# Optimization experiments

Measured on AMD Instinct MI355X. Metric: run time of the kernel, lower is better.

## Reference

```python
import jax, jax.numpy as jnp
import numpy as np

LN_EPS = 1e-5


def setup_inputs() -> dict:
    key = jax.random.key(0)
    ks = jax.random.split(key, 8)
    dim = 256
    b, n3 = 8, 6144  # seq dim holds 3 concatenated token streams of n=2048 each
    s = 0.02
    return {
        "x": jax.random.normal(ks[0], (b, n3, dim), jnp.float32),
        "ln_g": jnp.ones((dim,), jnp.float32),
        "ln_b": jnp.zeros((dim,), jnp.float32),
        "Wq": jax.random.normal(ks[1], (dim, dim), jnp.float32) * s,
        "bq": jax.random.normal(ks[2], (dim,), jnp.float32) * s,
        "Wk": jax.random.normal(ks[3], (dim, dim), jnp.float32) * s,
        "bk": jax.random.normal(ks[4], (dim,), jnp.float32) * s,
        "Wv": jax.random.normal(ks[5], (dim, dim), jnp.float32) * s,
        "bv": jax.random.normal(ks[6], (dim,), jnp.float32) * s,
        "Wo": jax.random.normal(ks[7], (dim, dim), jnp.float32) * s,
        "bo": jnp.zeros((dim,), jnp.float32),
        "heads": 8,
    }


def reference(x, ln_g, ln_b, Wq, bq, Wk, bk, Wv, bv, Wo, bo, heads):
    dim = x.shape[-1]
    scale = dim ** (-0.5)  # NOTE: full dim, as in the original module
    d = dim // heads

    def cross_attn(xcat):
        # LayerNorm over last dim (applied to concatenated [2b, n, dim])
        mu = jnp.mean(xcat, axis=-1, keepdims=True)
        var = jnp.mean(jnp.square(xcat - mu), axis=-1, keepdims=True)
        xn = (xcat - mu) * jax.lax.rsqrt(var + LN_EPS) * ln_g + ln_b
        x1, x2 = jnp.split(xn, 2, axis=0)  # queries from stream 1, kv from stream 2
        q = x1 @ Wq.T + bq
        k = x2 @ Wk.T + bk
        v = x2 @ Wv.T + bv
        b_, n_ = q.shape[0], q.shape[1]
        q = q.reshape(b_, n_, heads, d).transpose(0, 2, 1, 3)  # b h n d
        k = k.reshape(b_, n_, heads, d).transpose(0, 2, 1, 3)
        v = v.reshape(b_, n_, heads, d).transpose(0, 2, 1, 3)
        dots = jnp.einsum('bhid,bhjd->bhij', q, k) * scale
        attn = jax.nn.softmax(dots, axis=-1)
        out = jnp.einsum('bhij,bhjd->bhid', attn, v)
        out = out.transpose(0, 2, 1, 3).reshape(b_, n_, dim)
        return out @ Wo.T + bo  # dropout is identity in eval

    x_origin, x_emap, x_lbp = jnp.split(x, 3, axis=1)
    out_oe = cross_attn(jnp.concatenate((x_origin, x_emap), axis=0))
    out_ol = cross_attn(jnp.concatenate((x_origin, x_lbp), axis=0))
    return out_oe + out_ol
```

## Files before the change

### kernel.cpp

```cpp
#include <hip/hip_runtime.h>
#include <hip/hip_bf16.h>
#include <math.h>

#define LN_EPS 1e-5f
#define QSCALE 0.09016844005556021f

typedef __attribute__((ext_vector_type(8))) short short8;
typedef __attribute__((ext_vector_type(4))) short short4v;
typedef __attribute__((ext_vector_type(4))) float f32x4;
typedef __attribute__((ext_vector_type(16))) float f32x16;

__device__ inline ushort f2bf(float f) {
  __hip_bfloat16 h = __float2bfloat16(f);
  return *reinterpret_cast<ushort*>(&h);
}

__device__ inline uint pk2bf(float a, float b) {
  uint ua = __float_as_uint(a) + 0x8000u;
  uint ub = __float_as_uint(b) + 0x8000u;
  return __builtin_amdgcn_perm(ub, ua, 0x07060302u);
}


__global__ __launch_bounds__(256) void ln_wcast_kernel(
    const float* __restrict__ x, const float* __restrict__ lng,
    const float* __restrict__ lnb,
    const float* __restrict__ Wq, const float* __restrict__ Wk,
    const float* __restrict__ Wv, const float* __restrict__ Wo,
    ushort* __restrict__ xn, ushort* __restrict__ wbf) {
  if (blockIdx.x < 256) {
    int t = blockIdx.x * 256 + threadIdx.x;
    int e0 = t * 4;
    int m = e0 >> 16, off = e0 & 65535;
    const float* src = (m == 0) ? Wq : (m == 1) ? Wk : (m == 2) ? Wv : Wo;
    float4 v = *(const float4*)(src + off);
    ushort4 o;
    o.x = f2bf(v.x); o.y = f2bf(v.y); o.z = f2bf(v.z); o.w = f2bf(v.w);
    *(ushort4*)(wbf + m * 65536 + off) = o;
    return;
  }
  int w = threadIdx.x >> 6;
  int lane = threadIdx.x & 63;
  size_t token = (size_t)(blockIdx.x - 256) * 4 + w;
  float4 v = *(const float4*)(x + token * 256 + lane * 4);
  float s  = v.x + v.y + v.z + v.w;
  float s2 = v.x * v.x + v.y * v.y + v.z * v.z + v.w * v.w;
#pragma unroll
  for (int off = 32; off >= 1; off >>= 1) {
    s  += __shfl_xor(s, off, 64);
    s2 += __shfl_xor(s2, off, 64);
  }
  float mu  = s * (1.0f / 256.0f);
  float var = s2 * (1.0f / 256.0f) - mu * mu;
  float rs  = rsqrtf(var + LN_EPS);
  float4 g = *(const float4*)(lng + lane * 4);
  float4 bb = *(const float4*)(lnb + lane * 4);
  ushort4 o;
  o.x = f2bf((v.x - mu) * rs * g.x + bb.x);
  o.y = f2bf((v.y - mu) * rs * g.y + bb.y);
  o.z = f2bf((v.z - mu) * rs * g.z + bb.z);
  o.w = f2bf((v.w - mu) * rs * g.w + bb.w);
  *(ushort4*)(xn + token * 256 + lane * 4) = o;
}

__global__ __launch_bounds__(256) void proj_kernel(
    const ushort* __restrict__ xn,
    const ushort* __restrict__ wq, const ushort* __restrict__ wk,
    const ushort* __restrict__ wv,
    const float* __restrict__ bq, const float* __restrict__ bk,
    const float* __restrict__ bv,
    ushort* __restrict__ qb, ushort* __restrict__ keb, ushort* __restrict__ vTe,
    ushort* __restrict__ klb, ushort* __restrict__ vTl) {
  int z = blockIdx.z;
  int tid = threadIdx.x;
  int w = tid >> 6, lane = tid & 63;
  int n = lane & 15, quad = lane >> 4;
  int cbase = blockIdx.y * 128 + w * 32;
  int b = (blockIdx.x * 128) >> 11;
  int r0 = (blockIdx.x * 128) & 2047;

  if (z == 0) {
    const ushort* xbase = xn + ((size_t)b * 6144 + r0) * 256;
    short8 wf[2][8];
#pragma unroll
    for (int ct = 0; ct < 2; ++ct)
#pragma unroll
      for (int kc = 0; kc < 8; ++kc)
        wf[ct][kc] = *(const short8*)(wq + (size_t)(cbase + ct * 16 + n) * 256 + kc * 32 + quad * 8);
    float4 bt[2];
    bt[0] = *(const float4*)(bq + cbase + quad * 4);
    bt[1] = *(const float4*)(bq + cbase + 16 + quad * 4);

    short8 xfA[8], xfB[8];
#pragma unroll
    for (int kc = 0; kc < 8; ++kc)
      xfA[kc] = *(const short8*)(xbase + (size_t)n * 256 + kc * 32 + quad * 8);

#pragma unroll
    for (int tt = 0; tt < 8; ++tt) {
      const short8* cur = (tt & 1) ? xfB : xfA;
      short8* nxt = (tt & 1) ? xfA : xfB;
      if (tt < 7) {
#pragma unroll
        for (int kc = 0; kc < 8; ++kc)
          nxt[kc] = *(const short8*)(xbase + (size_t)((tt + 1) * 16 + n) * 256 + kc * 32 + quad * 8);
      }
      f32x4 acc[2] = {{0.f, 0.f, 0.f, 0.f}, {0.f, 0.f, 0.f, 0.f}};
#pragma unroll
      for (int ct = 0; ct < 2; ++ct)
#pragma unroll
        for (int kc = 0; kc < 8; ++kc)
          acc[ct] = __builtin_amdgcn_mfma_f32_16x16x32_bf16(wf[ct][kc], cur[kc], acc[ct], 0, 0, 0);
      int n2 = r0 + tt * 16 + n;
#pragma unroll
      for (int ct = 0; ct < 2; ++ct) {
        int c = cbase + ct * 16 + quad * 4;
        int h = c >> 5, d = c & 31;
        float* bp = (float*)&bt[ct];
        ushort4 st;
        st.x = f2bf((acc[ct][0] + bp[0]) * QSCALE);
        st.y = f2bf((acc[ct][1] + bp[1]) * QSCALE);
        st.z = f2bf((acc[ct][2] + bp[2]) * QSCALE);
        st.w = f2bf((acc[ct][3] + bp[3]) * QSCALE);
        *(ushort4*)(qb + (((size_t)(b * 8 + h) * 2048) + n2) * 32 + d) = st;
      }
    }
  } else {
    int s = z;
    ushort* kout = (z == 1) ? keb : klb;
    ushort* vout = (z == 1) ? vTe : vTl;
    const ushort* xbase = xn + ((size_t)b * 6144 + s * 2048 + r0) * 256;
    short8 wfk[2][8], wfv[2][8];
#pragma unroll
    for (int ct = 0; ct < 2; ++ct)
#pragma unroll
      for (int kc = 0; kc < 8; ++kc) {
        wfk[ct][kc] = *(const short8*)(wk + (size_t)(cbase + ct * 16 + n) * 256 + kc * 32 + quad * 8);
        wfv[ct][kc] = *(const short8*)(wv + (size_t)(cbase + ct * 16 + n) * 256 + kc * 32 + quad * 8);
      }
    float4 btk[2];
    btk[0] = *(const float4*)(bk + cbase + quad * 4);
    btk[1] = *(const float4*)(bk + cbase + 16 + quad * 4);
    float bsv[2] = {bv[cbase + n], bv[cbase + 16 + n]};

    short8 xfA[8], xfB[8];
#pragma unroll
    for (int kc = 0; kc < 8; ++kc)
      xfA[kc] = *(const short8*)(xbase + (size_t)n * 256 + kc * 32 + quad * 8);

#pragma unroll
    for (int tt = 0; tt < 8; ++tt) {
      const short8* cur = (tt & 1) ? xfB : xfA;
      short8* nxt = (tt & 1) ? xfA : xfB;
      if (tt < 7) {
#pragma unroll
        for (int kc = 0; kc < 8; ++kc)
          nxt[kc] = *(const short8*)(xbase + (size_t)((tt + 1) * 16 + n) * 256 + kc * 32 + quad * 8);
      }
      f32x4 ack[2] = {{0.f, 0.f, 0.f, 0.f}, {0.f, 0.f, 0.f, 0.f}};
      f32x4 acv[2] = {{0.f, 0.f, 0.f, 0.f}, {0.f, 0.f, 0.f, 0.f}};
#pragma unroll
      for (int ct = 0; ct < 2; ++ct)
#pragma unroll
        for (int kc = 0; kc < 8; ++kc) {
          ack[ct] = __builtin_amdgcn_mfma_f32_16x16x32_bf16(wfk[ct][kc], cur[kc], ack[ct], 0, 0, 0);
          acv[ct] = __builtin_amdgcn_mfma_f32_16x16x32_bf16(cur[kc], wfv[ct][kc], acv[ct], 0, 0, 0);
        }
      int n2 = r0 + tt * 16 + n;
#pragma unroll
      for (int ct = 0; ct < 2; ++ct) {
        int c = cbase + ct * 16 + quad * 4;
        int h = c >> 5, d = c & 31;
        float* bp = (float*)&btk[ct];
        ushort4 st;
        st.x = f2bf(ack[ct][0] + bp[0]);
        st.y = f2bf(ack[ct][1] + bp[1]);
        st.z = f2bf(ack[ct][2] + bp[2]);
        st.w = f2bf(ack[ct][3] + bp[3]);
        *(ushort4*)(kout + (((size_t)(b * 8 + h) * 2048) + n2) * 32 + d) = st;
      }
      int tq = r0 + tt * 16 + quad * 4;
      int ktile = tq >> 5;
      int u = (tq >> 4) & 1;
      int i0 = 4 * (quad >> 1);
      int hi2 = quad & 1;
#pragma unroll
      for (int ct = 0; ct < 2; ++ct) {
        int c = cbase + ct * 16 + n;
        int h = c >> 5;
        int d = ct * 16 + n;
        int lane2 = d + 32 * hi2;
        ushort4 st;
        st.x = f2bf(acv[ct][0] + bsv[ct]);
        st.y = f2bf(acv[ct][1] + bsv[ct]);
        st.z = f2bf(acv[ct][2] + bsv[ct]);
        st.w = f2bf(acv[ct][3] + bsv[ct]);
        *(ushort4*)(vout + (size_t)(b * 8 + h) * 65536
                    + ktile * 1024 + u * 512 + lane2 * 8 + i0) = st;
      }
    }
  }
}

__global__ __launch_bounds__(256, 3) void attn_kernel(
    const ushort* __restrict__ q,
    const ushort* __restrict__ ke, const ushort* __restrict__ vTe,
    const ushort* __restrict__ kl, const ushort* __restrict__ vTl,
    ushort* __restrict__ osum_e, ushort* __restrict__ osum_l) {
  int tid = threadIdx.x;
  int w = tid >> 6, lane = tid & 63;
  int l31 = lane & 31, hi = lane >> 5;

  union { uint4 uu; short8 s8; } one_u;
  one_u.uu.x = 0x3F803F80u; one_u.uu.y = 0x3F803F80u;
  one_u.uu.z = 0x3F803F80u; one_u.uu.w = 0x3F803F80u;
  const short8 vone8 = one_u.s8;

  int L = blockIdx.y * 8 + blockIdx.x;
  int xcd = L & 7, idx = L >> 3;
  int bh = (idx >> 5) * 8 + xcd;
  int rem = idx & 31;
  int s = rem >> 4;
  int q0 = (rem & 15) * 128;
  int qbase = q0 + w * 32;

  const ushort* K  = (s == 0 ? ke : kl) + (size_t)bh * 65536;
  const ushort* VT = (s == 0 ? vTe : vTl) + (size_t)bh * 65536;
  ushort* osum = (s == 0) ? osum_e : osum_l;

  short8 qf[2];
#pragma unroll
  for (int sl = 0; sl < 2; ++sl)
    qf[sl] = *(const short8*)(q + ((size_t)bh * 2048 + qbase + l31) * 32 + sl * 16 + hi * 8);

  f32x16 zero16;
#pragma unroll
  for (int r = 0; r < 16; ++r) zero16[r] = 0.f;
  f32x16 oacc = zero16;
  f32x16 lacc = zero16;

  auto loadKV = [&](short8* kf, short8* vf, int jt) {
    const ushort* kb = K + (size_t)jt * 2048;
#pragma unroll
    for (int kt = 0; kt < 2; ++kt)
#pragma unroll
      for (int sl = 0; sl < 2; ++sl)
        kf[kt * 2 + sl] = *(const short8*)(kb + (kt * 32 + l31) * 32 + sl * 16 + hi * 8);
    const ushort* vb = VT + (size_t)jt * 2048 + lane * 8;
#pragma unroll
    for (int m = 0; m < 4; ++m)
      vf[m] = *(const short8*)(vb + m * 512);
  };

  auto compute = [&](const short8* kf, const short8* vf) {
#pragma unroll
    for (int kt = 0; kt < 2; ++kt) {
      __builtin_amdgcn_s_setprio(1);
      f32x16 sacc = __builtin_amdgcn_mfma_f32_32x32x16_bf16(kf[kt * 2 + 0], qf[0], zero16, 0, 0, 0);
      sacc = __builtin_amdgcn_mfma_f32_32x32x16_bf16(kf[kt * 2 + 1], qf[1], sacc, 0, 0, 0);
      __builtin_amdgcn_s_setprio(0);
      float p[16];
#pragma unroll
      for (int r = 0; r < 16; ++r) p[r] = __builtin_amdgcn_exp2f(sacc[r]);
      short8 pa[2];
#pragma unroll
      for (int u = 0; u < 2; ++u) {
        union { uint4 uu; short8 s8; } cv;
        cv.uu.x = pk2bf(p[8 * u + 0], p[8 * u + 1]);
        cv.uu.y = pk2bf(p[8 * u + 2], p[8 * u + 3]);
        cv.uu.z = pk2bf(p[8 * u + 4], p[8 * u + 5]);
        cv.uu.w = pk2bf(p[8 * u + 6], p[8 * u + 7]);
        pa[u] = cv.s8;
      }
      __builtin_amdgcn_s_setprio(1);
      oacc = __builtin_amdgcn_mfma_f32_32x32x16_bf16(pa[0], vf[kt * 2 + 0], oacc, 0, 0, 0);
      oacc = __builtin_amdgcn_mfma_f32_32x32x16_bf16(pa[1], vf[kt * 2 + 1], oacc, 0, 0, 0);
      lacc = __builtin_amdgcn_mfma_f32_32x32x16_bf16(pa[0], vone8, lacc, 0, 0, 0);
      lacc = __builtin_amdgcn_mfma_f32_32x32x16_bf16(pa[1], vone8, lacc, 0, 0, 0);
      __builtin_amdgcn_s_setprio(0);
    }
  };

  short8 kfA[4], kfB[4], vfA[4], vfB[4];
  loadKV(kfA, vfA, 0);
  for (int jt = 0; jt < 32; jt += 2) {
    loadKV(kfB, vfB, jt + 1);
    compute(kfA, vfA);
    if (jt + 2 < 32) loadKV(kfA, vfA, jt + 2);
    compute(kfB, vfB);
  }

  int b = bh >> 3, h = bh & 7;
#pragma unroll
  for (int r = 0; r < 16; ++r) {
    int qr = (r & 3) + 8 * (r >> 2) + 4 * hi;
    float invr = __builtin_amdgcn_rcpf(lacc[r]);
    float v = oacc[r] * invr;
    size_t row = (size_t)b * 2048 + qbase + qr;
    osum[row * 256 + h * 32 + l31] = f2bf(v);
  }
}

__global__ __launch_bounds__(256) void outproj_kernel(
    const ushort* __restrict__ ose, const ushort* __restrict__ osl,
    const ushort* __restrict__ wo,
    const float* __restrict__ bo, float* __restrict__ out) {
  int tid = threadIdx.x;
  int w = tid >> 6, lane = tid & 63;
  int n = lane & 15, quad = lane >> 4;
  int cbase = blockIdx.y * 128 + w * 32;

  short8 wfrag[2][8];
#pragma unroll
  for (int ct = 0; ct < 2; ++ct)
#pragma unroll
    for (int kc = 0; kc < 8; ++kc)
      wfrag[ct][kc] = *(const short8*)(wo + (size_t)(cbase + ct * 16 + n) * 256 + kc * 32 + quad * 8);
  float4 bt[2];
  bt[0] = *(const float4*)(bo + cbase + quad * 4);
  bt[1] = *(const float4*)(bo + cbase + 16 + quad * 4);

  const ushort* ae = ose + (size_t)(blockIdx.x * 64) * 256;
  const ushort* al = osl + (size_t)(blockIdx.x * 64) * 256;

#pragma unroll
  for (int tt = 0; tt < 4; ++tt) {
    short8 xe[8], xl[8];
#pragma unroll
    for (int kc = 0; kc < 8; ++kc)
      xe[kc] = *(const short8*)(ae + (size_t)(tt * 16 + n) * 256 + kc * 32 + quad * 8);
#pragma unroll
    for (int kc = 0; kc < 8; ++kc)
      xl[kc] = *(const short8*)(al + (size_t)(tt * 16 + n) * 256 + kc * 32 + quad * 8);

    int tok = blockIdx.x * 64 + tt * 16 + n;
    f32x4 acc[2] = {{0.f, 0.f, 0.f, 0.f}, {0.f, 0.f, 0.f, 0.f}};
#pragma unroll
    for (int ct = 0; ct < 2; ++ct)
#pragma unroll
      for (int kc = 0; kc < 8; ++kc)
        acc[ct] = __builtin_amdgcn_mfma_f32_16x16x32_bf16(wfrag[ct][kc], xe[kc], acc[ct], 0, 0, 0);
#pragma unroll
    for (int ct = 0; ct < 2; ++ct)
#pragma unroll
      for (int kc = 0; kc < 8; ++kc)
        acc[ct] = __builtin_amdgcn_mfma_f32_16x16x32_bf16(wfrag[ct][kc], xl[kc], acc[ct], 0, 0, 0);
#pragma unroll
    for (int ct = 0; ct < 2; ++ct) {
      int c = cbase + ct * 16 + quad * 4;
      float* bp = (float*)&bt[ct];
      float4 st;
      st.x = acc[ct][0] + 2.0f * bp[0];
      st.y = acc[ct][1] + 2.0f * bp[1];
      st.z = acc[ct][2] + 2.0f * bp[2];
      st.w = acc[ct][3] + 2.0f * bp[3];
      *(float4*)(out + (size_t)tok * 256 + c) = st;
    }
  }
}

extern "C" void kernel_launch(void* const* d_in, const int* in_sizes, int n_in,
                              void* d_out, int out_size, void* d_ws, size_t ws_size,
                              hipStream_t stream) {
  const float* x   = (const float*)d_in[0];
  const float* lng = (const float*)d_in[1];
  const float* lnb = (const float*)d_in[2];
  const float* Wq  = (const float*)d_in[3];
  const float* bq  = (const float*)d_in[4];
  const float* Wk  = (const float*)d_in[5];
  const float* bk  = (const float*)d_in[6];
  const float* Wv  = (const float*)d_in[7];
  const float* bv  = (const float*)d_in[8];
  const float* Wo  = (const float*)d_in[9];
  const float* bo  = (const float*)d_in[10];
  float* out = (float*)d_out;

  ushort* ws = (ushort*)d_ws;
  const size_t XN  = (size_t)49152 * 256;
  const size_t QKV = (size_t)64 * 2048 * 32;
  ushort* xn     = ws;
  ushort* wbf    = xn + XN;
  ushort* qb     = wbf + 4 * 65536;
  ushort* keb    = qb  + QKV;
  ushort* vTe    = keb + QKV;
  ushort* klb    = vTe + QKV;
  ushort* vTl    = klb + QKV;
  ushort* osum_e = vTl + QKV;
  ushort* osum_l = xn;

  hipLaunchKernelGGL(ln_wcast_kernel, dim3(12544), dim3(256), 0, stream,
                     x, lng, lnb, Wq, Wk, Wv, Wo, xn, wbf);
  hipLaunchKernelGGL(proj_kernel, dim3(128, 2, 3), dim3(256), 0, stream,
                     xn, wbf, wbf + 65536, wbf + 131072, bq, bk, bv,
                     qb, keb, vTe, klb, vTl);
  hipLaunchKernelGGL(attn_kernel, dim3(8, 256), dim3(256), 0, stream,
                     qb, keb, vTe, klb, vTl, osum_e, osum_l);
  hipLaunchKernelGGL(outproj_kernel, dim3(256, 2), dim3(256), 0, stream,
                     osum_e, osum_l, wbf + 196608, bo, out);
}
```

Before: 273.6 us.

## Fuse LayerNorm into projection kernel and fold gamma/beta into weights

```diff
diff --git a/kernel.cpp b/kernel.cpp
--- a/kernel.cpp
+++ b/kernel.cpp
@@ -22,53 +22,48 @@
 }
 
 
-__global__ __launch_bounds__(256) void ln_wcast_kernel(
-    const float* __restrict__ x, const float* __restrict__ lng,
-    const float* __restrict__ lnb,
+__global__ __launch_bounds__(256) void wcast_kernel(
     const float* __restrict__ Wq, const float* __restrict__ Wk,
     const float* __restrict__ Wv, const float* __restrict__ Wo,
-    ushort* __restrict__ xn, ushort* __restrict__ wbf) {
-  if (blockIdx.x < 256) {
-    int t = blockIdx.x * 256 + threadIdx.x;
-    int e0 = t * 4;
-    int m = e0 >> 16, off = e0 & 65535;
-    const float* src = (m == 0) ? Wq : (m == 1) ? Wk : (m == 2) ? Wv : Wo;
-    float4 v = *(const float4*)(src + off);
-    ushort4 o;
-    o.x = f2bf(v.x); o.y = f2bf(v.y); o.z = f2bf(v.z); o.w = f2bf(v.w);
-    *(ushort4*)(wbf + m * 65536 + off) = o;
-    return;
-  }
-  int w = threadIdx.x >> 6;
-  int lane = threadIdx.x & 63;
-  size_t token = (size_t)(blockIdx.x - 256) * 4 + w;
-  float4 v = *(const float4*)(x + token * 256 + lane * 4);
-  float s  = v.x + v.y + v.z + v.w;
-  float s2 = v.x * v.x + v.y * v.y + v.z * v.z + v.w * v.w;
-#pragma unroll
-  for (int off = 32; off >= 1; off >>= 1) {
-    s  += __shfl_xor(s, off, 64);
-    s2 += __shfl_xor(s2, off, 64);
-  }
-  float mu  = s * (1.0f / 256.0f);
-  float var = s2 * (1.0f / 256.0f) - mu * mu;
-  float rs  = rsqrtf(var + LN_EPS);
-  float4 g = *(const float4*)(lng + lane * 4);
-  float4 bb = *(const float4*)(lnb + lane * 4);
+    const float* __restrict__ lng, const float* __restrict__ lnb,
+    const float* __restrict__ bq, const float* __restrict__ bk,
+    const float* __restrict__ bv,
+    ushort* __restrict__ wbf, float* __restrict__ bqp,
+    float* __restrict__ bkp, float* __restrict__ bvp) {
+  int w = threadIdx.x >> 6, lane = threadIdx.x & 63;
+  int m = blockIdx.x >> 6;
+  int c = (blockIdx.x & 63) * 4 + w;
+  const float* W = (m == 0) ? Wq : (m == 1) ? Wk : (m == 2) ? Wv : Wo;
+  float4 wr = *(const float4*)(W + (size_t)c * 256 + lane * 4);
+  float dot = 0.f;
+  if (m < 3) {
+    float4 g  = *(const float4*)(lng + lane * 4);
+    float4 lb = *(const float4*)(lnb + lane * 4);
+    dot = wr.x * lb.x + wr.y * lb.y + wr.z * lb.z + wr.w * lb.w;
+    wr.x *= g.x; wr.y *= g.y; wr.z *= g.z; wr.w *= g.w;
+  }
+  float scale = (m == 0) ? QSCALE : 1.f;
+  wr.x *= scale; wr.y *= scale; wr.z *= scale; wr.w *= scale;
   ushort4 o;
-  o.x = f2bf((v.x - mu) * rs * g.x + bb.x);
-  o.y = f2bf((v.y - mu) * rs * g.y + bb.y);
-  o.z = f2bf((v.z - mu) * rs * g.z + bb.z);
-  o.w = f2bf((v.w - mu) * rs * g.w + bb.w);
-  *(ushort4*)(xn + token * 256 + lane * 4) = o;
+  o.x = f2bf(wr.x); o.y = f2bf(wr.y); o.z = f2bf(wr.z); o.w = f2bf(wr.w);
+  *(ushort4*)(wbf + m * 65536 + (size_t)c * 256 + lane * 4) = o;
+  if (m < 3) {
+#pragma unroll
+    for (int off = 32; off >= 1; off >>= 1) dot += __shfl_xor(dot, off, 64);
+    if (lane == 0) {
+      float base = ((m == 0) ? bq : (m == 1) ? bk : bv)[c];
+      float bb = (base + dot) * scale;
+      ((m == 0) ? bqp : (m == 1) ? bkp : bvp)[c] = bb;
+    }
+  }
 }
 
 __global__ __launch_bounds__(256) void proj_kernel(
-    const ushort* __restrict__ xn,
+    const float* __restrict__ x,
     const ushort* __restrict__ wq, const ushort* __restrict__ wk,
     const ushort* __restrict__ wv,
-    const float* __restrict__ bq, const float* __restrict__ bk,
-    const float* __restrict__ bv,
+    const float* __restrict__ bqp, const float* __restrict__ bkp,
+    const float* __restrict__ bvp,
     ushort* __restrict__ qb, ushort* __restrict__ keb, ushort* __restrict__ vTe,
     ushort* __restrict__ klb, ushort* __restrict__ vTl) {
   int z = blockIdx.z;
@@ -78,9 +73,55 @@
   int cbase = blockIdx.y * 128 + w * 32;
   int b = (blockIdx.x * 128) >> 11;
   int r0 = (blockIdx.x * 128) & 2047;
+  int s = (z == 0) ? 0 : z;
+  const float* xbase = x + ((size_t)b * 6144 + (size_t)s * 2048 + r0) * 256;
+
+  float4 fr[16];
+  short8 xb[8];
+
+  auto loadX = [&](int tt) {
+    const float* rp = xbase + (size_t)(tt * 16 + n) * 256 + quad * 8;
+#pragma unroll
+    for (int kc = 0; kc < 8; ++kc) {
+      fr[kc * 2]     = *(const float4*)(rp + kc * 32);
+      fr[kc * 2 + 1] = *(const float4*)(rp + kc * 32 + 4);
+    }
+  };
+  auto lnconv = [&]() {
+    float4 a0 = fr[0] + fr[1],  a1 = fr[2] + fr[3];
+    float4 a2 = fr[4] + fr[5],  a3 = fr[6] + fr[7];
+    float4 a4 = fr[8] + fr[9],  a5 = fr[10] + fr[11];
+    float4 a6 = fr[12] + fr[13], a7 = fr[14] + fr[15];
+    float4 b0 = (a0 + a1) + (a2 + a3);
+    float4 b1 = (a4 + a5) + (a6 + a7);
+    float4 sv = b0 + b1;
+    float ssum = (sv.x + sv.y) + (sv.z + sv.w);
+    float4 q0 = fr[0]*fr[0] + fr[1]*fr[1],   q1 = fr[2]*fr[2] + fr[3]*fr[3];
+    float4 q2 = fr[4]*fr[4] + fr[5]*fr[5],   q3 = fr[6]*fr[6] + fr[7]*fr[7];
+    float4 q4 = fr[8]*fr[8] + fr[9]*fr[9],   q5 = fr[10]*fr[10] + fr[11]*fr[11];
+    float4 q6 = fr[12]*fr[12] + fr[13]*fr[13], q7 = fr[14]*fr[14] + fr[15]*fr[15];
+    float4 qv = ((q0 + q1) + (q2 + q3)) + ((q4 + q5) + (q6 + q7));
+    float s2 = (qv.x + qv.y) + (qv.z + qv.w);
+    ssum += __shfl_xor(ssum, 16, 64);
+    ssum += __shfl_xor(ssum, 32, 64);
+    s2   += __shfl_xor(s2, 16, 64);
+    s2   += __shfl_xor(s2, 32, 64);
+    float mu  = ssum * (1.0f / 256.0f);
+    float var = s2 * (1.0f / 256.0f) - mu * mu;
+    float rs  = rsqrtf(var + LN_EPS);
+    float nmr = -mu * rs;
+    const float* pf = (const float*)fr;
+#pragma unroll
+    for (int kc = 0; kc < 8; ++kc) {
+      union { ushort u[8]; short8 s8; } cv;
+#pragma unroll
+      for (int j = 0; j < 8; ++j)
+        cv.u[j] = f2bf(fmaf(pf[kc * 8 + j], rs, nmr));
+      xb[kc] = cv.s8;
+    }
+  };
 
   if (z == 0) {
-    const ushort* xbase = xn + ((size_t)b * 6144 + r0) * 256;
     short8 wf[2][8];
 #pragma unroll
     for (int ct = 0; ct < 2; ++ct)
@@ -88,29 +129,20 @@
       for (int kc = 0; kc < 8; ++kc)
         wf[ct][kc] = *(const short8*)(wq + (size_t)(cbase + ct * 16 + n) * 256 + kc * 32 + quad * 8);
     float4 bt[2];
-    bt[0] = *(const float4*)(bq + cbase + quad * 4);
-    bt[1] = *(const float4*)(bq + cbase + 16 + quad * 4);
-
-    short8 xfA[8], xfB[8];
-#pragma unroll
-    for (int kc = 0; kc < 8; ++kc)
-      xfA[kc] = *(const short8*)(xbase + (size_t)n * 256 + kc * 32 + quad * 8);
-
+    bt[0] = *(const float4*)(bqp + cbase + quad * 4);
+    bt[1] = *(const float4*)(bqp + cbase + 16 + quad * 4);
+
+    loadX(0);
+    lnconv();
 #pragma unroll
     for (int tt = 0; tt < 8; ++tt) {
-      const short8* cur = (tt & 1) ? xfB : xfA;
-      short8* nxt = (tt & 1) ? xfA : xfB;
-      if (tt < 7) {
+      if (tt < 7) loadX(tt + 1);
+      f32x4 acc[2] = {{0.f, 0.f, 0.f, 0.f}, {0.f, 0.f, 0.f, 0.f}};
+#pragma unroll
+      for (int ct = 0; ct < 2; ++ct)
 #pragma unroll
         for (int kc = 0; kc < 8; ++kc)
-          nxt[kc] = *(const short8*)(xbase + (size_t)((tt + 1) * 16 + n) * 256 + kc * 32 + quad * 8);
-      }
-      f32x4 acc[2] = {{0.f, 0.f, 0.f, 0.f}, {0.f, 0.f, 0.f, 0.f}};
-#pragma unroll
-      for (int ct = 0; ct < 2; ++ct)
-#pragma unroll
-        for (int kc = 0; kc < 8; ++kc)
-          acc[ct] = __builtin_amdgcn_mfma_f32_16x16x32_bf16(wf[ct][kc], cur[kc], acc[ct], 0, 0, 0);
+          acc[ct] = __builtin_amdgcn_mfma_f32_16x16x32_bf16(wf[ct][kc], xb[kc], acc[ct], 0, 0, 0);
       int n2 = r0 + tt * 16 + n;
 #pragma unroll
       for (int ct = 0; ct < 2; ++ct) {
@@ -118,18 +150,17 @@
         int h = c >> 5, d = c & 31;
         float* bp = (float*)&bt[ct];
         ushort4 st;
-        st.x = f2bf((acc[ct][0] + bp[0]) * QSCALE);
-        st.y = f2bf((acc[ct][1] + bp[1]) * QSCALE);
-        st.z = f2bf((acc[ct][2] + bp[2]) * QSCALE);
-        st.w = f2bf((acc[ct][3] + bp[3]) * QSCALE);
+        st.x = f2bf(acc[ct][0] + bp[0]);
+        st.y = f2bf(acc[ct][1] + bp[1]);
+        st.z = f2bf(acc[ct][2] + bp[2]);
+        st.w = f2bf(acc[ct][3] + bp[3]);
         *(ushort4*)(qb + (((size_t)(b * 8 + h) * 2048) + n2) * 32 + d) = st;
       }
+      if (tt < 7) lnconv();
     }
   } else {
-    int s = z;
     ushort* kout = (z == 1) ? keb : klb;
     ushort* vout = (z == 1) ? vTe : vTl;
-    const ushort* xbase = xn + ((size_t)b * 6144 + s * 2048 + r0) * 256;
     short8 wfk[2][8], wfv[2][8];
 #pragma unroll
     for (int ct = 0; ct < 2; ++ct)
@@ -139,32 +170,23 @@
         wfv[ct][kc] = *(const short8*)(wv + (size_t)(cbase + ct * 16 + n) * 256 + kc * 32 + quad * 8);
       }
     float4 btk[2];
-    btk[0] = *(const float4*)(bk + cbase + quad * 4);
-    btk[1] = *(const float4*)(bk + cbase + 16 + quad * 4);
-    float bsv[2] = {bv[cbase + n], bv[cbase + 16 + n]};
-
-    short8 xfA[8], xfB[8];
-#pragma unroll
-    for (int kc = 0; kc < 8; ++kc)
-      xfA[kc] = *(const short8*)(xbase + (size_t)n * 256 + kc * 32 + quad * 8);
-
+    btk[0] = *(const float4*)(bkp + cbase + quad * 4);
+    btk[1] = *(const float4*)(bkp + cbase + 16 + quad * 4);
+    float bsv[2] = {bvp[cbase + n], bvp[cbase + 16 + n]};
+
+    loadX(0);
+    lnconv();
 #pragma unroll
     for (int tt = 0; tt < 8; ++tt) {
-      const short8* cur = (tt & 1) ? xfB : xfA;
-      short8* nxt = (tt & 1) ? xfA : xfB;
-      if (tt < 7) {
-#pragma unroll
-        for (int kc = 0; kc < 8; ++kc)
-          nxt[kc] = *(const short8*)(xbase + (size_t)((tt + 1) * 16 + n) * 256 + kc * 32 + quad * 8);
-      }
+      if (tt < 7) loadX(tt + 1);
       f32x4 ack[2] = {{0.f, 0.f, 0.f, 0.f}, {0.f, 0.f, 0.f, 0.f}};
       f32x4 acv[2] = {{0.f, 0.f, 0.f, 0.f}, {0.f, 0.f, 0.f, 0.f}};
 #pragma unroll
       for (int ct = 0; ct < 2; ++ct)
 #pragma unroll
         for (int kc = 0; kc < 8; ++kc) {
-          ack[ct] = __builtin_amdgcn_mfma_f32_16x16x32_bf16(wfk[ct][kc], cur[kc], ack[ct], 0, 0, 0);
-          acv[ct] = __builtin_amdgcn_mfma_f32_16x16x32_bf16(cur[kc], wfv[ct][kc], acv[ct], 0, 0, 0);
+          ack[ct] = __builtin_amdgcn_mfma_f32_16x16x32_bf16(wfk[ct][kc], xb[kc], ack[ct], 0, 0, 0);
+          acv[ct] = __builtin_amdgcn_mfma_f32_16x16x32_bf16(xb[kc], wfv[ct][kc], acv[ct], 0, 0, 0);
         }
       int n2 = r0 + tt * 16 + n;
 #pragma unroll
@@ -198,6 +220,7 @@
         *(ushort4*)(vout + (size_t)(b * 8 + h) * 65536
                     + ktile * 1024 + u * 512 + lane2 * 8 + i0) = st;
       }
+      if (tt < 7) lnconv();
     }
   }
 }
@@ -376,22 +399,23 @@
   float* out = (float*)d_out;
 
   ushort* ws = (ushort*)d_ws;
-  const size_t XN  = (size_t)49152 * 256;
   const size_t QKV = (size_t)64 * 2048 * 32;
-  ushort* xn     = ws;
-  ushort* wbf    = xn + XN;
+  ushort* wbf    = ws;
   ushort* qb     = wbf + 4 * 65536;
   ushort* keb    = qb  + QKV;
   ushort* vTe    = keb + QKV;
   ushort* klb    = vTe + QKV;
   ushort* vTl    = klb + QKV;
   ushort* osum_e = vTl + QKV;
-  ushort* osum_l = xn;
-
-  hipLaunchKernelGGL(ln_wcast_kernel, dim3(12544), dim3(256), 0, stream,
-                     x, lng, lnb, Wq, Wk, Wv, Wo, xn, wbf);
+  ushort* osum_l = osum_e + QKV;
+  float*  bqp    = (float*)(osum_l + QKV);
+  float*  bkp    = bqp + 256;
+  float*  bvp    = bkp + 256;
+
+  hipLaunchKernelGGL(wcast_kernel, dim3(256), dim3(256), 0, stream,
+                     Wq, Wk, Wv, Wo, lng, lnb, bq, bk, bv, wbf, bqp, bkp, bvp);
   hipLaunchKernelGGL(proj_kernel, dim3(128, 2, 3), dim3(256), 0, stream,
-                     xn, wbf, wbf + 65536, wbf + 131072, bq, bk, bv,
+                     x, wbf, wbf + 65536, wbf + 131072, bqp, bkp, bvp,
                      qb, keb, vTe, klb, vTl);
   hipLaunchKernelGGL(attn_kernel, dim3(8, 256), dim3(256), 0, stream,
                      qb, keb, vTe, klb, vTl, osum_e, osum_l);
```

Result: slower. 293.4 us (+7.2%).
